# Performance work log

Hardware: AMD Instinct MI355X
Metric: run time of the kernel (lower is better)

The kernel has to match this reference:

```python
import jax, jax.numpy as jnp
import numpy as np

B, L, K = 2, 2048, 48
NUM_RBF = 16
NUM_POS = 16      # positional embedding dim
MAX_REL = 32      # max relative sequence offset
EDGE = 128        # edge feature dim
N_ATOMS = 5       # Ca, N, C, O, virtual Cb -> 25 atom pairs
EDGE_IN = NUM_POS + N_ATOMS * N_ATOMS * NUM_RBF  # 16 + 400 = 416


def setup_inputs() -> dict:
    key = jax.random.key(0)
    ks = jax.random.split(key, 6)
    # backbone coords (N, CA, C, O); scaled so pairwise distances span the RBF range [2, 22]
    X = jax.random.normal(ks[0], (B, L, 4, 3), dtype=jnp.float32) * 5.0
    mask = jnp.ones((B, L), dtype=jnp.float32)
    residue_idx = jnp.broadcast_to(jnp.arange(L, dtype=jnp.int32), (B, L))
    chain_labels = jnp.ones((B, L), dtype=jnp.int32)
    # learned params
    W_pos = jax.random.normal(ks[1], (2 * MAX_REL + 2, NUM_POS), dtype=jnp.float32) * 0.05
    b_pos = jnp.zeros((NUM_POS,), dtype=jnp.float32)
    W_edge = jax.random.normal(ks[2], (EDGE_IN, EDGE), dtype=jnp.float32) * 0.05  # no bias (ProteinMPNN)
    ln_gamma = jnp.ones((EDGE,), dtype=jnp.float32)
    ln_beta = jnp.zeros((EDGE,), dtype=jnp.float32)
    return {"X": X, "mask": mask, "residue_idx": residue_idx, "chain_labels": chain_labels,
            "W_pos": W_pos, "b_pos": b_pos, "W_edge": W_edge,
            "ln_gamma": ln_gamma, "ln_beta": ln_beta}


def _gather_nodes(nodes, e_idx):
    # nodes: [B, L, C], e_idx: [B, L, K] -> [B, L, K, C]
    b, l, k = e_idx.shape
    flat = e_idx.reshape(b, l * k)
    return jnp.take_along_axis(nodes, flat[..., None], axis=1).reshape(b, l, k, nodes.shape[-1])


def reference(X, mask, residue_idx, chain_labels, W_pos, b_pos, W_edge, ln_gamma, ln_beta):
    b, l = mask.shape
    k = min(K, l)
    N_at, Ca, C_at, O_at = X[:, :, 0], X[:, :, 1], X[:, :, 2], X[:, :, 3]

    # ---- kNN over Ca distances (masked) ----
    mask_2d = mask[:, :, None] * mask[:, None, :]
    dX = Ca[:, None, :, :] - Ca[:, :, None, :]            # [B, L, L, 3]
    D = mask_2d * jnp.sqrt(jnp.sum(dX * dX, -1) + 1e-6)    # [B, L, L]
    D_max = jnp.max(D, -1, keepdims=True)
    D_adjust = D + (1.0 - mask_2d) * D_max
    _, E_idx = jax.lax.top_k(-D_adjust, k)                 # k smallest distances -> [B, L, K]

    # ---- virtual Cb ----
    bb = Ca - N_at
    cc = C_at - Ca
    aa = jnp.cross(bb, cc)
    Cb = -0.58273431 * aa + 0.56802827 * bb - 0.54067466 * cc + Ca

    # ---- 25 pairwise atom-atom RBFs ----
    atoms = jnp.stack([Ca, N_at, C_at, O_at, Cb], axis=-2)            # [B, L, 5, 3]
    atoms_nb = _gather_nodes(atoms.reshape(b, l, N_ATOMS * 3), E_idx)  # [B, L, K, 15]
    atoms_nb = atoms_nb.reshape(b, l, k, N_ATOMS, 3)
    diff = atoms[:, :, None, :, None, :] - atoms_nb[:, :, :, None, :, :]  # [B, L, K, 5, 5, 3]
    Dp = jnp.sqrt(jnp.sum(diff * diff, -1) + 1e-6)                        # [B, L, K, 5, 5]
    mu = jnp.linspace(2.0, 22.0, NUM_RBF)
    sigma = (22.0 - 2.0) / NUM_RBF
    RBF_all = jnp.exp(-jnp.square((Dp[..., None] - mu) / sigma))          # [B, L, K, 5, 5, 16]
    RBF_all = RBF_all.reshape(b, l, k, N_ATOMS * N_ATOMS * NUM_RBF)       # [B, L, K, 400]

    # ---- relative positional encoding ----
    flat = E_idx.reshape(b, l * k)
    ridx_nb = jnp.take_along_axis(residue_idx, flat, axis=1).reshape(b, l, k)
    offset = residue_idx[:, :, None] - ridx_nb                            # [B, L, K]
    chain_nb = jnp.take_along_axis(chain_labels, flat, axis=1).reshape(b, l, k)
    same_chain = (chain_labels[:, :, None] == chain_nb).astype(jnp.int32)
    d = jnp.clip(offset + MAX_REL, 0, 2 * MAX_REL) * same_chain + (1 - same_chain) * (2 * MAX_REL + 1)
    d_onehot = jax.nn.one_hot(d, 2 * MAX_REL + 2, dtype=RBF_all.dtype)    # [B, L, K, 66]
    E_positional = d_onehot @ W_pos + b_pos                                # [B, L, K, 16]

    # ---- edge embedding + LayerNorm ----
    E = jnp.concatenate([E_positional, RBF_all], axis=-1) @ W_edge         # [B, L, K, 128]
    m = jnp.mean(E, -1, keepdims=True)
    v = jnp.mean(jnp.square(E - m), -1, keepdims=True)
    E = (E - m) * jax.lax.rsqrt(v + 1e-5) * ln_gamma + ln_beta
    return E, E_idx
```

## Files before the change

kernel.cpp:

```cpp
#include <hip/hip_runtime.h>
#include <hip/hip_bf16.h>
#include <stdint.h>

#define BB 2
#define LL 2048
#define KNN 48
#define MAXREL 32
#define EDGE_D 128
#define FSTRIDE 232
#define FLOFF   11136
#define WFH_ELEMS 53248
#define EIDX_BYTES (BB*LL*KNN*4)

typedef unsigned long long u64;
typedef __bf16 bf16_t;
typedef bf16_t bf16x8 __attribute__((ext_vector_type(8)));
typedef float f32x4 __attribute__((ext_vector_type(4)));

union U16x8 { uint4 q; bf16x8 v; };

__device__ __forceinline__ u64 u64min(u64 a, u64 b) { return a < b ? a : b; }

__device__ __forceinline__ u64 shfl_xor_u64(u64 v, int m) {
    unsigned lo = __shfl_xor((unsigned)(v & 0xffffffffull), m);
    unsigned hi = __shfl_xor((unsigned)(v >> 32), m);
    return (((u64)hi) << 32) | lo;
}

__device__ __forceinline__ void split_hi_lo(float f, unsigned short& h, unsigned short& l) {
    unsigned bits = __float_as_uint(f);
    h = (unsigned short)(bits >> 16);
    float hf = __uint_as_float(bits & 0xffff0000u);
    float lo = f - hf;
    l = (unsigned short)(__float_as_uint(lo) >> 16);
}

__global__ __launch_bounds__(256) void prep_kernel(const float* __restrict__ W,
                                                   unsigned short* __restrict__ Wf)
{
    int tid = blockIdx.x * 256 + threadIdx.x;
    if (tid >= WFH_ELEMS) return;
    int e    = tid & 7;
    int lane = (tid >> 3) & 63;
    int nt   = (tid >> 9) & 7;
    int ktg  = tid >> 12;
    int k    = ktg * 32 + ((lane >> 4) << 3) + e;
    int col  = (nt << 4) + (lane & 15);
    float f  = W[k * 128 + col];
    unsigned short h, l;
    split_hi_lo(f, h, l);
    Wf[tid]             = h;
    Wf[tid + WFH_ELEMS] = l;
}

__global__ __launch_bounds__(256) void knn_kernel(
    const float* __restrict__ X, const float* __restrict__ mask,
    int* __restrict__ eidx_i, float* __restrict__ eidx_f)
{
    const int bi   = blockIdx.x;
    const int b    = bi >> 11;
    const int i    = bi & (LL - 1);
    const int tid  = threadIdx.x;
    const int wv   = tid >> 6;
    const int lane = tid & 63;

    __shared__ int   hist[256];
    __shared__ int   ctrl[4];
    __shared__ int   cnt;
    __shared__ u64   list[64];
    __shared__ float wsh[4];
    __shared__ u64   wmin[2][4];

    const float* Xb = X + (size_t)b * LL * 12;
    const float* mb = mask + (size_t)b * LL;

    const float cax = Xb[i * 12 + 3];
    const float cay = Xb[i * 12 + 4];
    const float caz = Xb[i * 12 + 5];
    const float mi  = mb[i];

    float D[8], M2[8];
    float dmax = 0.0f;

    #pragma unroll
    for (int t = 0; t < 8; t++) {
        int j = (t << 8) + tid;
        float dx = Xb[j * 12 + 3] - cax;
        float dy = Xb[j * 12 + 4] - cay;
        float dz = Xb[j * 12 + 5] - caz;
        float s  = __fadd_rn(__fadd_rn(__fmul_rn(dx, dx), __fmul_rn(dy, dy)),
                             __fmul_rn(dz, dz));
        float m2 = __fmul_rn(mi, mb[j]);
        float d  = __fmul_rn(m2, sqrtf(__fadd_rn(s, 1e-6f)));
        D[t]  = d;
        M2[t] = m2;
        dmax  = fmaxf(dmax, d);
    }

    hist[tid] = 0;
    if (tid == 0) cnt = 0;

    #pragma unroll
    for (int off = 32; off; off >>= 1) dmax = fmaxf(dmax, __shfl_xor(dmax, off));
    if (lane == 0) wsh[wv] = dmax;
    __syncthreads();
    dmax = fmaxf(fmaxf(wsh[0], wsh[1]), fmaxf(wsh[2], wsh[3]));

    u64 key[8];
    #pragma unroll
    for (int t = 0; t < 8; t++) {
        int j = (t << 8) + tid;
        float dadj = __fadd_rn(D[t], __fmul_rn(1.0f - M2[t], dmax));
        key[t] = (((u64)__float_as_uint(dadj)) << 32) | (unsigned)j;
        atomicAdd(&hist[(int)(key[t] >> 55)], 1);
    }
    __syncthreads();

    if (wv == 0) {
        int h0 = hist[4 * lane], h1 = hist[4 * lane + 1];
        int h2 = hist[4 * lane + 2], h3 = hist[4 * lane + 3];
        int s = h0 + h1 + h2 + h3;
        int sc = s;
        #pragma unroll
        for (int off = 1; off < 64; off <<= 1) {
            int o = __shfl_up(sc, off);
            if (lane >= off) sc += o;
        }
        u64 ball = __ballot(sc >= KNN);
        int fl = __ffsll((unsigned long long)ball) - 1;
        if (lane == fl) {
            int cb = sc - s;
            int B, cbB;
            if      (cb + h0 >= KNN)           { B = 4 * lane;     cbB = cb; }
            else if (cb + h0 + h1 >= KNN)      { B = 4 * lane + 1; cbB = cb + h0; }
            else if (cb + h0 + h1 + h2 >= KNN) { B = 4 * lane + 2; cbB = cb + h0 + h1; }
            else                               { B = 4 * lane + 3; cbB = cb + h0 + h1 + h2; }
            ctrl[0] = B; ctrl[1] = cbB;
        }
    }
    __syncthreads();
    const int B = ctrl[0], cbB = ctrl[1];
    hist[tid] = 0;
    __syncthreads();

    #pragma unroll
    for (int t = 0; t < 8; t++) {
        if ((int)(key[t] >> 55) == B)
            atomicAdd(&hist[(int)(key[t] >> 47) & 255], 1);
    }
    __syncthreads();

    if (wv == 0) {
        const int T2 = KNN - cbB;
        int h0 = hist[4 * lane], h1 = hist[4 * lane + 1];
        int h2 = hist[4 * lane + 2], h3 = hist[4 * lane + 3];
        int s = h0 + h1 + h2 + h3;
        int sc = s;
        #pragma unroll
        for (int off = 1; off < 64; off <<= 1) {
            int o = __shfl_up(sc, off);
            if (lane >= off) sc += o;
        }
        u64 ball = __ballot(sc >= T2);
        int fl = __ffsll((unsigned long long)ball) - 1;
        if (lane == fl) {
            int cb = sc - s;
            int B2, cum;
            if      (cb + h0 >= T2)           { B2 = 4 * lane;     cum = cb + h0; }
            else if (cb + h0 + h1 >= T2)      { B2 = 4 * lane + 1; cum = cb + h0 + h1; }
            else if (cb + h0 + h1 + h2 >= T2) { B2 = 4 * lane + 2; cum = cb + h0 + h1 + h2; }
            else                              { B2 = 4 * lane + 3; cum = cb + h0 + h1 + h2 + h3; }
            ctrl[2] = B2; ctrl[3] = cbB + cum;
        }
    }
    __syncthreads();
    const int B2 = ctrl[2], m = ctrl[3];

    if (m <= 64) {
        #pragma unroll
        for (int t = 0; t < 8; t++) {
            int b1 = (int)(key[t] >> 55);
            int b2 = (int)(key[t] >> 47) & 255;
            if (b1 < B || (b1 == B && b2 <= B2)) {
                int p = atomicAdd(&cnt, 1);
                list[p] = key[t];
            }
        }
        __syncthreads();

        if (wv == 0) {
            u64 v = (lane < m) ? list[lane] : ~0ull;
            #pragma unroll
            for (int k = 2; k <= 64; k <<= 1) {
                #pragma unroll
                for (int j = k >> 1; j > 0; j >>= 1) {
                    u64 o = shfl_xor_u64(v, j);
                    bool takemin = (((lane & k) == 0) == ((lane & j) == 0));
                    u64 mn = u64min(v, o);
                    u64 mx = v ^ o ^ mn;
                    v = takemin ? mn : mx;
                }
            }
            if (lane < KNN) {
                int j = (int)(v & 0xffffffffu);
                eidx_i[(size_t)bi * KNN + lane] = j;
                eidx_f[(size_t)bi * KNN + lane] = (float)j;
            }
        }
    } else {
        for (int s = 0; s < KNN; s++) {
            u64 lmin = key[0];
            #pragma unroll
            for (int t = 1; t < 8; t++) lmin = u64min(lmin, key[t]);
            #pragma unroll
            for (int off = 1; off < 64; off <<= 1) lmin = u64min(lmin, shfl_xor_u64(lmin, off));
            if (lane == 0) wmin[s & 1][wv] = lmin;
            __syncthreads();
            u64 gmin = u64min(u64min(wmin[s & 1][0], wmin[s & 1][1]),
                              u64min(wmin[s & 1][2], wmin[s & 1][3]));
            if (tid == 0) {
                int j = (int)(gmin & 0xffffffffu);
                eidx_i[(size_t)bi * KNN + s] = j;
                eidx_f[(size_t)bi * KNN + s] = (float)j;
            }
            #pragma unroll
            for (int t = 0; t < 8; t++) if (key[t] == gmin) key[t] = ~0ull;
        }
    }
}

__global__ __launch_bounds__(512) void edge_kernel(
    const float* __restrict__ X,
    const int*   __restrict__ ridx, const int* __restrict__ chain,
    const float* __restrict__ Wpos, const float* __restrict__ bpos,
    const unsigned short* __restrict__ Wf,
    const float* __restrict__ gamma, const float* __restrict__ beta,
    const int*   __restrict__ eidx_i, float* __restrict__ Eout)
{
    __shared__ __align__(16) unsigned short fHL[2 * 48 * FSTRIDE];
    __shared__ float nbat[48][5][3];
    __shared__ float ctr[5][3];
    __shared__ int   dsel[48];
    __shared__ int   nbi[48];
    __shared__ float sumP[48][8];
    __shared__ float sqP[48][8];
    __shared__ float lnM[48], lnR[48];

    const int bi   = blockIdx.x;
    const int b    = bi >> 11;
    const int i    = bi & (LL - 1);
    const int tid  = threadIdx.x;
    const int w    = tid >> 6;
    const int lane = tid & 63;
    const float* Xb = X + (size_t)b * LL * 12;

    if (tid < 48) {
        int j = eidx_i[(size_t)bi * KNN + tid];
        nbi[tid] = j;
        int off = ridx[b * LL + i] - ridx[b * LL + j];
        int sc  = (chain[b * LL + i] == chain[b * LL + j]);
        int d   = off + MAXREL;
        d = d < 0 ? 0 : (d > 2 * MAXREL ? 2 * MAXREL : d);
        dsel[tid] = sc ? d : (2 * MAXREL + 1);
    }
    if (tid >= 448 && tid < 452) {
        int a = tid - 448;
        int src = (a == 0) ? 1 : ((a == 1) ? 0 : a);
        ctr[a][0] = Xb[i * 12 + src * 3 + 0];
        ctr[a][1] = Xb[i * 12 + src * 3 + 1];
        ctr[a][2] = Xb[i * 12 + src * 3 + 2];
    }
    __syncthreads();

    if (tid < 192) {
        int e = tid >> 2, a = tid & 3;
        int src = (a == 0) ? 1 : ((a == 1) ? 0 : a);
        int j = nbi[e];
        nbat[e][a][0] = Xb[j * 12 + src * 3 + 0];
        nbat[e][a][1] = Xb[j * 12 + src * 3 + 1];
        nbat[e][a][2] = Xb[j * 12 + src * 3 + 2];
    }
    __syncthreads();

    if (tid < 48) {
        float bx = nbat[tid][0][0] - nbat[tid][1][0];
        float by = nbat[tid][0][1] - nbat[tid][1][1];
        float bz = nbat[tid][0][2] - nbat[tid][1][2];
        float cx = nbat[tid][2][0] - nbat[tid][0][0];
        float cy = nbat[tid][2][1] - nbat[tid][0][1];
        float cz = nbat[tid][2][2] - nbat[tid][0][2];
        float ax = by * cz - bz * cy;
        float ay = bz * cx - bx * cz;
        float az = bx * cy - by * cx;
        nbat[tid][4][0] = -0.58273431f * ax + 0.56802827f * bx - 0.54067466f * cx + nbat[tid][0][0];
        nbat[tid][4][1] = -0.58273431f * ay + 0.56802827f * by - 0.54067466f * cy + nbat[tid][0][1];
        nbat[tid][4][2] = -0.58273431f * az + 0.56802827f * bz - 0.54067466f * cz + nbat[tid][0][2];
    } else if (tid == 48) {
        float bx = ctr[0][0] - ctr[1][0];
        float by = ctr[0][1] - ctr[1][1];
        float bz = ctr[0][2] - ctr[1][2];
        float cx = ctr[2][0] - ctr[0][0];
        float cy = ctr[2][1] - ctr[0][1];
        float cz = ctr[2][2] - ctr[0][2];
        float ax = by * cz - bz * cy;
        float ay = bz * cx - bx * cz;
        float az = bx * cy - by * cx;
        ctr[4][0] = -0.58273431f * ax + 0.56802827f * bx - 0.54067466f * cx + ctr[0][0];
        ctr[4][1] = -0.58273431f * ay + 0.56802827f * by - 0.54067466f * cy + ctr[0][1];
        ctr[4][2] = -0.58273431f * az + 0.56802827f * bz - 0.54067466f * cz + ctr[0][2];
    }
    __syncthreads();

    for (int idx = tid; idx < 48 * 16; idx += 512) {
        int e = idx >> 4, p = idx & 15;
        float f = Wpos[dsel[e] * 16 + p] + bpos[p];
        unsigned short h, l;
        split_hi_lo(f, h, l);
        fHL[e * FSTRIDE + p]         = h;
        fHL[FLOFF + e * FSTRIDE + p] = l;
    }
    for (int idx = tid; idx < 48 * 16; idx += 512) {
        int e = idx >> 4, pr = idx & 15;
        if (pr < 13) {
            int A = pr / 5, Bv = pr % 5;
            int klocal = 16 + pr * 16;
            float dx = ctr[A][0] - nbat[e][Bv][0];
            float dy = ctr[A][1] - nbat[e][Bv][1];
            float dz = ctr[A][2] - nbat[e][Bv][2];
            float d  = sqrtf(dx * dx + dy * dy + dz * dz + 1e-6f);
            uint hw[8], lw[8];
            #pragma unroll
            for (int rp = 0; rp < 8; rp++) {
                float mu0 = 2.0f + 1.3333334f * (float)(2 * rp);
                float mu1 = 2.0f + 1.3333334f * (float)(2 * rp + 1);
                float t0 = (d - mu0) * 0.8f, t1 = (d - mu1) * 0.8f;
                float v0 = __expf(-t0 * t0), v1 = __expf(-t1 * t1);
                unsigned short h0, l0, h1, l1;
                split_hi_lo(v0, h0, l0); split_hi_lo(v1, h1, l1);
                hw[rp] = (uint)h0 | ((uint)h1 << 16);
                lw[rp] = (uint)l0 | ((uint)l1 << 16);
            }
            uint4* dh = (uint4*)&fHL[e * FSTRIDE + klocal];
            dh[0] = make_uint4(hw[0], hw[1], hw[2], hw[3]);
            dh[1] = make_uint4(hw[4], hw[5], hw[6], hw[7]);
            uint4* dl = (uint4*)&fHL[FLOFF + e * FSTRIDE + klocal];
            dl[0] = make_uint4(lw[0], lw[1], lw[2], lw[3]);
            dl[1] = make_uint4(lw[4], lw[5], lw[6], lw[7]);
        }
    }
    __syncthreads();

    const unsigned short* aB = &fHL[(lane & 15) * FSTRIDE + ((lane >> 4) << 3)];
    const unsigned short* wB = Wf + (size_t)w * 512 + (size_t)lane * 8;
    f32x4 acc0 = {0.f, 0.f, 0.f, 0.f}, acc1 = acc0, acc2 = acc0;

    #pragma unroll
    for (int kt = 0; kt < 7; kt++) {
        U16x8 wh, wl, a0h, a1h, a2h, a0l, a1l, a2l;
        wh.q  = *(const uint4*)(wB + kt * 4096);
        wl.q  = *(const uint4*)(wB + WFH_ELEMS + kt * 4096);
        a0h.q = *(const uint4*)(aB + kt * 32);
        a1h.q = *(const uint4*)(aB + 16 * FSTRIDE + kt * 32);
        a2h.q = *(const uint4*)(aB + 32 * FSTRIDE + kt * 32);
        a0l.q = *(const uint4*)(aB + FLOFF + kt * 32);
        a1l.q = *(const uint4*)(aB + FLOFF + 16 * FSTRIDE + kt * 32);
        a2l.q = *(const uint4*)(aB + FLOFF + 32 * FSTRIDE + kt * 32);
        acc0 = __builtin_amdgcn_mfma_f32_16x16x32_bf16(a0h.v, wh.v, acc0, 0, 0, 0);
        acc1 = __builtin_amdgcn_mfma_f32_16x16x32_bf16(a1h.v, wh.v, acc1, 0, 0, 0);
        acc2 = __builtin_amdgcn_mfma_f32_16x16x32_bf16(a2h.v, wh.v, acc2, 0, 0, 0);
        acc0 = __builtin_amdgcn_mfma_f32_16x16x32_bf16(a0l.v, wh.v, acc0, 0, 0, 0);
        acc1 = __builtin_amdgcn_mfma_f32_16x16x32_bf16(a1l.v, wh.v, acc1, 0, 0, 0);
        acc2 = __builtin_amdgcn_mfma_f32_16x16x32_bf16(a2l.v, wh.v, acc2, 0, 0, 0);
        acc0 = __builtin_amdgcn_mfma_f32_16x16x32_bf16(a0h.v, wl.v, acc0, 0, 0, 0);
        acc1 = __builtin_amdgcn_mfma_f32_16x16x32_bf16(a1h.v, wl.v, acc1, 0, 0, 0);
        acc2 = __builtin_amdgcn_mfma_f32_16x16x32_bf16(a2h.v, wl.v, acc2, 0, 0, 0);
    }
    __syncthreads();

    for (int idx = tid; idx < 48 * 16; idx += 512) {
        int e = idx >> 4, prl = idx & 15;
        if (prl < 12) {
            int pr = 13 + prl;
            int A = pr / 5, Bv = pr % 5;
            int klocal = prl * 16;
            float dx = ctr[A][0] - nbat[e][Bv][0];
            float dy = ctr[A][1] - nbat[e][Bv][1];
            float dz = ctr[A][2] - nbat[e][Bv][2];
            float d  = sqrtf(dx * dx + dy * dy + dz * dz + 1e-6f);
            uint hw[8], lw[8];
            #pragma unroll
            for (int rp = 0; rp < 8; rp++) {
                float mu0 = 2.0f + 1.3333334f * (float)(2 * rp);
                float mu1 = 2.0f + 1.3333334f * (float)(2 * rp + 1);
                float t0 = (d - mu0) * 0.8f, t1 = (d - mu1) * 0.8f;
                float v0 = __expf(-t0 * t0), v1 = __expf(-t1 * t1);
                unsigned short h0, l0, h1, l1;
                split_hi_lo(v0, h0, l0); split_hi_lo(v1, h1, l1);
                hw[rp] = (uint)h0 | ((uint)h1 << 16);
                lw[rp] = (uint)l0 | ((uint)l1 << 16);
            }
            uint4* dh = (uint4*)&fHL[e * FSTRIDE + klocal];
            dh[0] = make_uint4(hw[0], hw[1], hw[2], hw[3]);
            dh[1] = make_uint4(hw[4], hw[5], hw[6], hw[7]);
            uint4* dl = (uint4*)&fHL[FLOFF + e * FSTRIDE + klocal];
            dl[0] = make_uint4(lw[0], lw[1], lw[2], lw[3]);
            dl[1] = make_uint4(lw[4], lw[5], lw[6], lw[7]);
        }
    }
    __syncthreads();

    #pragma unroll
    for (int kt = 0; kt < 6; kt++) {
        U16x8 wh, wl, a0h, a1h, a2h, a0l, a1l, a2l;
        wh.q  = *(const uint4*)(wB + (7 + kt) * 4096);
        wl.q  = *(const uint4*)(wB + WFH_ELEMS + (7 + kt) * 4096);
        a0h.q = *(const uint4*)(aB + kt * 32);
        a1h.q = *(const uint4*)(aB + 16 * FSTRIDE + kt * 32);
        a2h.q = *(const uint4*)(aB + 32 * FSTRIDE + kt * 32);
        a0l.q = *(const uint4*)(aB + FLOFF + kt * 32);
        a1l.q = *(const uint4*)(aB + FLOFF + 16 * FSTRIDE + kt * 32);
        a2l.q = *(const uint4*)(aB + FLOFF + 32 * FSTRIDE + kt * 32);
        acc0 = __builtin_amdgcn_mfma_f32_16x16x32_bf16(a0h.v, wh.v, acc0, 0, 0, 0);
        acc1 = __builtin_amdgcn_mfma_f32_16x16x32_bf16(a1h.v, wh.v, acc1, 0, 0, 0);
        acc2 = __builtin_amdgcn_mfma_f32_16x16x32_bf16(a2h.v, wh.v, acc2, 0, 0, 0);
        acc0 = __builtin_amdgcn_mfma_f32_16x16x32_bf16(a0l.v, wh.v, acc0, 0, 0, 0);
        acc1 = __builtin_amdgcn_mfma_f32_16x16x32_bf16(a1l.v, wh.v, acc1, 0, 0, 0);
        acc2 = __builtin_amdgcn_mfma_f32_16x16x32_bf16(a2l.v, wh.v, acc2, 0, 0, 0);
        acc0 = __builtin_amdgcn_mfma_f32_16x16x32_bf16(a0h.v, wl.v, acc0, 0, 0, 0);
        acc1 = __builtin_amdgcn_mfma_f32_16x16x32_bf16(a1h.v, wl.v, acc1, 0, 0, 0);
        acc2 = __builtin_amdgcn_mfma_f32_16x16x32_bf16(a2h.v, wl.v, acc2, 0, 0, 0);
    }

    {
        float vals[3][4] = {{acc0[0], acc0[1], acc0[2], acc0[3]},
                            {acc1[0], acc1[1], acc1[2], acc1[3]},
                            {acc2[0], acc2[1], acc2[2], acc2[3]}};
        #pragma unroll
        for (int mt = 0; mt < 3; mt++) {
            #pragma unroll
            for (int r = 0; r < 4; r++) {
                float sm = vals[mt][r], sq = sm * sm;
                #pragma unroll
                for (int off = 1; off < 16; off <<= 1) {
                    sm += __shfl_xor(sm, off);
                    sq += __shfl_xor(sq, off);
                }
                if ((lane & 15) == 0) {
                    int row = mt * 16 + ((lane >> 4) << 2) + r;
                    sumP[row][w] = sm;
                    sqP[row][w]  = sq;
                }
            }
        }
        __syncthreads();
        if (tid < 48) {
            float s = 0.f, q = 0.f;
            #pragma unroll
            for (int t = 0; t < 8; t++) { s += sumP[tid][t]; q += sqP[tid][t]; }
            float m = s * 0.0078125f;
            lnM[tid] = m;
            lnR[tid] = rsqrtf(q * 0.0078125f - m * m + 1e-5f);
        }
        __syncthreads();

        const int col = (w << 4) + (lane & 15);
        const float g  = gamma[col];
        const float bt = beta[col];
        float* Eo = Eout + (size_t)bi * KNN * EDGE_D;
        #pragma unroll
        for (int mt = 0; mt < 3; mt++) {
            #pragma unroll
            for (int r = 0; r < 4; r++) {
                int row = mt * 16 + ((lane >> 4) << 2) + r;
                Eo[(size_t)row * EDGE_D + col] =
                    (vals[mt][r] - lnM[row]) * lnR[row] * g + bt;
            }
        }
    }
}

extern "C" void kernel_launch(void* const* d_in, const int* in_sizes, int n_in,
                              void* d_out, int out_size, void* d_ws, size_t ws_size,
                              hipStream_t stream) {
    const float* X     = (const float*)d_in[0];
    const float* mask  = (const float*)d_in[1];
    const int*   ridx  = (const int*)d_in[2];
    const int*   chain = (const int*)d_in[3];
    const float* Wpos  = (const float*)d_in[4];
    const float* bpos  = (const float*)d_in[5];
    const float* Wedge = (const float*)d_in[6];
    const float* gamma = (const float*)d_in[7];
    const float* beta  = (const float*)d_in[8];

    float* out    = (float*)d_out;
    float* Eout   = out;
    float* eidx_f = out + (size_t)BB * LL * KNN * EDGE_D;
    int*   eidx_i = (int*)d_ws;
    unsigned short* Wf = (unsigned short*)((char*)d_ws + EIDX_BYTES);

    hipLaunchKernelGGL(prep_kernel, dim3((WFH_ELEMS + 255) / 256), dim3(256), 0, stream,
                       Wedge, Wf);
    hipLaunchKernelGGL(knn_kernel, dim3(BB * LL), dim3(256), 0, stream,
                       X, mask, eidx_i, eidx_f);
    hipLaunchKernelGGL(edge_kernel, dim3(BB * LL), dim3(512), 0, stream,
                       X, ridx, chain, Wpos, bpos, Wf, gamma, beta, eidx_i, Eout);
}
```

Before: 242.3 us.

## Bin kNN histogram by value range, fragment-major LDS, prefetch weights

The kNN selection now builds its first histogram over the linear range [dmin, dmax] of adjusted distances rather than over float exponent bits. The aim is that the first pass isolates the 48 nearest directly, without the second refinement pass or the serial fallback. The edge kernel stores A operands in LDS in a fragment-major layout with padding, so each lane's MFMA load is one contiguous uint4 with fewer bank conflicts. Weight fragments are prefetched one k-step ahead in registers, and launch bounds request higher occupancy. These changes add an extra min reduction and more register pressure, and binning by float value could behave differently on unusual distributions.

```diff
diff --git a/kernel.cpp b/kernel.cpp
--- a/kernel.cpp
+++ b/kernel.cpp
@@ -7,10 +7,11 @@
 #define KNN 48
 #define MAXREL 32
 #define EDGE_D 128
-#define FSTRIDE 232
-#define FLOFF   11136
 #define WFH_ELEMS 53248
 #define EIDX_BYTES (BB*LL*KNN*4)
+#define KT_PAD 65
+#define PM_FRAGS (7 * KT_PAD)
+#define TOT_FRAGS (2 * 3 * PM_FRAGS)
 
 typedef unsigned long long u64;
 typedef __bf16 bf16_t;
@@ -68,7 +69,7 @@
     __shared__ int   ctrl[4];
     __shared__ int   cnt;
     __shared__ u64   list[64];
-    __shared__ float wsh[4];
+    __shared__ float wshA[4], wshB[4];
     __shared__ u64   wmin[2][4];
 
     const float* Xb = X + (size_t)b * LL * 12;
@@ -102,17 +103,36 @@
 
     #pragma unroll
     for (int off = 32; off; off >>= 1) dmax = fmaxf(dmax, __shfl_xor(dmax, off));
-    if (lane == 0) wsh[wv] = dmax;
-    __syncthreads();
-    dmax = fmaxf(fmaxf(wsh[0], wsh[1]), fmaxf(wsh[2], wsh[3]));
+    if (lane == 0) wshA[wv] = dmax;
+    __syncthreads();
+    dmax = fmaxf(fmaxf(wshA[0], wshA[1]), fmaxf(wshA[2], wshA[3]));
 
     u64 key[8];
+    float dadj[8];
+    float dmin = 3.4e38f;
     #pragma unroll
     for (int t = 0; t < 8; t++) {
         int j = (t << 8) + tid;
-        float dadj = __fadd_rn(D[t], __fmul_rn(1.0f - M2[t], dmax));
-        key[t] = (((u64)__float_as_uint(dadj)) << 32) | (unsigned)j;
-        atomicAdd(&hist[(int)(key[t] >> 55)], 1);
+        float da = __fadd_rn(D[t], __fmul_rn(1.0f - M2[t], dmax));
+        dadj[t] = da;
+        key[t] = (((u64)__float_as_uint(da)) << 32) | (unsigned)j;
+        dmin = fminf(dmin, da);
+    }
+    #pragma unroll
+    for (int off = 32; off; off >>= 1) dmin = fminf(dmin, __shfl_xor(dmin, off));
+    if (lane == 0) wshB[wv] = dmin;
+    __syncthreads();
+    dmin = fminf(fminf(wshB[0], wshB[1]), fminf(wshB[2], wshB[3]));
+
+    const float range = dmax - dmin;
+    const float scale = (range > 1e-35f) ? (255.0f / range) : 0.0f;
+
+    int bin[8];
+    #pragma unroll
+    for (int t = 0; t < 8; t++) {
+        int bb = (int)((dadj[t] - dmin) * scale);
+        bin[t] = bb > 255 ? 255 : bb;
+        atomicAdd(&hist[bin[t]], 1);
     }
     __syncthreads();
 
@@ -130,68 +150,27 @@
         int fl = __ffsll((unsigned long long)ball) - 1;
         if (lane == fl) {
             int cb = sc - s;
-            int B, cbB;
-            if      (cb + h0 >= KNN)           { B = 4 * lane;     cbB = cb; }
-            else if (cb + h0 + h1 >= KNN)      { B = 4 * lane + 1; cbB = cb + h0; }
-            else if (cb + h0 + h1 + h2 >= KNN) { B = 4 * lane + 2; cbB = cb + h0 + h1; }
-            else                               { B = 4 * lane + 3; cbB = cb + h0 + h1 + h2; }
-            ctrl[0] = B; ctrl[1] = cbB;
-        }
-    }
-    __syncthreads();
-    const int B = ctrl[0], cbB = ctrl[1];
-    hist[tid] = 0;
-    __syncthreads();
-
-    #pragma unroll
-    for (int t = 0; t < 8; t++) {
-        if ((int)(key[t] >> 55) == B)
-            atomicAdd(&hist[(int)(key[t] >> 47) & 255], 1);
-    }
-    __syncthreads();
-
-    if (wv == 0) {
-        const int T2 = KNN - cbB;
-        int h0 = hist[4 * lane], h1 = hist[4 * lane + 1];
-        int h2 = hist[4 * lane + 2], h3 = hist[4 * lane + 3];
-        int s = h0 + h1 + h2 + h3;
-        int sc = s;
-        #pragma unroll
-        for (int off = 1; off < 64; off <<= 1) {
-            int o = __shfl_up(sc, off);
-            if (lane >= off) sc += o;
-        }
-        u64 ball = __ballot(sc >= T2);
-        int fl = __ffsll((unsigned long long)ball) - 1;
-        if (lane == fl) {
-            int cb = sc - s;
-            int B2, cum;
-            if      (cb + h0 >= T2)           { B2 = 4 * lane;     cum = cb + h0; }
-            else if (cb + h0 + h1 >= T2)      { B2 = 4 * lane + 1; cum = cb + h0 + h1; }
-            else if (cb + h0 + h1 + h2 >= T2) { B2 = 4 * lane + 2; cum = cb + h0 + h1 + h2; }
-            else                              { B2 = 4 * lane + 3; cum = cb + h0 + h1 + h2 + h3; }
-            ctrl[2] = B2; ctrl[3] = cbB + cum;
-        }
-    }
-    __syncthreads();
-    const int B2 = ctrl[2], m = ctrl[3];
-
-    if (m <= 64) {
+            int B, cbB, m1;
+            if      (cb + h0 >= KNN)           { B = 4*lane;   cbB = cb;          m1 = cb+h0; }
+            else if (cb + h0 + h1 >= KNN)      { B = 4*lane+1; cbB = cb+h0;       m1 = cb+h0+h1; }
+            else if (cb + h0 + h1 + h2 >= KNN) { B = 4*lane+2; cbB = cb+h0+h1;    m1 = cb+h0+h1+h2; }
+            else                               { B = 4*lane+3; cbB = cb+h0+h1+h2; m1 = cb+h0+h1+h2+h3; }
+            ctrl[0] = B; ctrl[1] = cbB; ctrl[2] = m1;
+        }
+    }
+    __syncthreads();
+    const int B = ctrl[0], cbB = ctrl[1], m1 = ctrl[2];
+
+    if (m1 <= 64) {
         #pragma unroll
         for (int t = 0; t < 8; t++) {
-            int b1 = (int)(key[t] >> 55);
-            int b2 = (int)(key[t] >> 47) & 255;
-            if (b1 < B || (b1 == B && b2 <= B2)) {
-                int p = atomicAdd(&cnt, 1);
-                list[p] = key[t];
-            }
+            if (bin[t] <= B) { int p = atomicAdd(&cnt, 1); list[p] = key[t]; }
         }
         __syncthreads();
-
         if (wv == 0) {
-            u64 v = (lane < m) ? list[lane] : ~0ull;
-            #pragma unroll
-            for (int k = 2; k <= 64; k <<= 1) {
+            u64 v = (lane < m1) ? list[lane] : ~0ull;
+            #pragma unroll
+            for (int k = 2; k <= 64; k <<= 1)
                 #pragma unroll
                 for (int j = k >> 1; j > 0; j >>= 1) {
                     u64 o = shfl_xor_u64(v, j);
@@ -200,36 +179,108 @@
                     u64 mx = v ^ o ^ mn;
                     v = takemin ? mn : mx;
                 }
-            }
             if (lane < KNN) {
                 int j = (int)(v & 0xffffffffu);
                 eidx_i[(size_t)bi * KNN + lane] = j;
                 eidx_f[(size_t)bi * KNN + lane] = (float)j;
             }
         }
-    } else {
-        for (int s = 0; s < KNN; s++) {
-            u64 lmin = key[0];
-            #pragma unroll
-            for (int t = 1; t < 8; t++) lmin = u64min(lmin, key[t]);
-            #pragma unroll
-            for (int off = 1; off < 64; off <<= 1) lmin = u64min(lmin, shfl_xor_u64(lmin, off));
-            if (lane == 0) wmin[s & 1][wv] = lmin;
-            __syncthreads();
-            u64 gmin = u64min(u64min(wmin[s & 1][0], wmin[s & 1][1]),
-                              u64min(wmin[s & 1][2], wmin[s & 1][3]));
-            if (tid == 0) {
-                int j = (int)(gmin & 0xffffffffu);
-                eidx_i[(size_t)bi * KNN + s] = j;
-                eidx_f[(size_t)bi * KNN + s] = (float)j;
-            }
-            #pragma unroll
-            for (int t = 0; t < 8; t++) if (key[t] == gmin) key[t] = ~0ull;
-        }
+        return;
+    }
+
+    hist[tid] = 0;
+    __syncthreads();
+    const float width  = range * (1.0f / 255.0f);
+    const float b_lo   = dmin + (float)B * width;
+    const float scale2 = (width > 1e-35f) ? (255.0f / width) : 0.0f;
+    int bin2[8];
+    #pragma unroll
+    for (int t = 0; t < 8; t++) {
+        if (bin[t] == B) {
+            int bb = (int)((dadj[t] - b_lo) * scale2);
+            bb = bb < 0 ? 0 : (bb > 255 ? 255 : bb);
+            bin2[t] = bb;
+            atomicAdd(&hist[bb], 1);
+        } else bin2[t] = 1 << 30;
+    }
+    __syncthreads();
+
+    if (wv == 0) {
+        const int T2 = KNN - cbB;
+        int h0 = hist[4 * lane], h1 = hist[4 * lane + 1];
+        int h2 = hist[4 * lane + 2], h3 = hist[4 * lane + 3];
+        int s = h0 + h1 + h2 + h3;
+        int sc = s;
+        #pragma unroll
+        for (int off = 1; off < 64; off <<= 1) {
+            int o = __shfl_up(sc, off);
+            if (lane >= off) sc += o;
+        }
+        u64 ball = __ballot(sc >= T2);
+        int fl = __ffsll((unsigned long long)ball) - 1;
+        if (lane == fl) {
+            int cb = sc - s;
+            int B2, cum;
+            if      (cb + h0 >= T2)           { B2 = 4*lane;   cum = cb+h0; }
+            else if (cb + h0 + h1 >= T2)      { B2 = 4*lane+1; cum = cb+h0+h1; }
+            else if (cb + h0 + h1 + h2 >= T2) { B2 = 4*lane+2; cum = cb+h0+h1+h2; }
+            else                              { B2 = 4*lane+3; cum = cb+h0+h1+h2+h3; }
+            ctrl[2] = B2; ctrl[3] = cbB + cum;
+        }
+    }
+    __syncthreads();
+    const int B2 = ctrl[2], m2 = ctrl[3];
+
+    if (m2 <= 64) {
+        #pragma unroll
+        for (int t = 0; t < 8; t++) {
+            if (bin[t] < B || (bin[t] == B && bin2[t] <= B2)) {
+                int p = atomicAdd(&cnt, 1); list[p] = key[t];
+            }
+        }
+        __syncthreads();
+        if (wv == 0) {
+            u64 v = (lane < m2) ? list[lane] : ~0ull;
+            #pragma unroll
+            for (int k = 2; k <= 64; k <<= 1)
+                #pragma unroll
+                for (int j = k >> 1; j > 0; j >>= 1) {
+                    u64 o = shfl_xor_u64(v, j);
+                    bool takemin = (((lane & k) == 0) == ((lane & j) == 0));
+                    u64 mn = u64min(v, o);
+                    u64 mx = v ^ o ^ mn;
+                    v = takemin ? mn : mx;
+                }
+            if (lane < KNN) {
+                int j = (int)(v & 0xffffffffu);
+                eidx_i[(size_t)bi * KNN + lane] = j;
+                eidx_f[(size_t)bi * KNN + lane] = (float)j;
+            }
+        }
+        return;
+    }
+
+    for (int s = 0; s < KNN; s++) {
+        u64 lmin = key[0];
+        #pragma unroll
+        for (int t = 1; t < 8; t++) lmin = u64min(lmin, key[t]);
+        #pragma unroll
+        for (int off = 1; off < 64; off <<= 1) lmin = u64min(lmin, shfl_xor_u64(lmin, off));
+        if (lane == 0) wmin[s & 1][wv] = lmin;
+        __syncthreads();
+        u64 gmin = u64min(u64min(wmin[s & 1][0], wmin[s & 1][1]),
+                          u64min(wmin[s & 1][2], wmin[s & 1][3]));
+        if (tid == 0) {
+            int j = (int)(gmin & 0xffffffffu);
+            eidx_i[(size_t)bi * KNN + s] = j;
+            eidx_f[(size_t)bi * KNN + s] = (float)j;
+        }
+        #pragma unroll
+        for (int t = 0; t < 8; t++) if (key[t] == gmin) key[t] = ~0ull;
     }
 }
 
-__global__ __launch_bounds__(512) void edge_kernel(
+__global__ __launch_bounds__(512, 6) void edge_kernel(
     const float* __restrict__ X,
     const int*   __restrict__ ridx, const int* __restrict__ chain,
     const float* __restrict__ Wpos, const float* __restrict__ bpos,
@@ -237,7 +288,7 @@
     const float* __restrict__ gamma, const float* __restrict__ beta,
     const int*   __restrict__ eidx_i, float* __restrict__ Eout)
 {
-    __shared__ __align__(16) unsigned short fHL[2 * 48 * FSTRIDE];
+    __shared__ __align__(16) uint4 frag[TOT_FRAGS];
     __shared__ float nbat[48][5][3];
     __shared__ float ctr[5][3];
     __shared__ int   dsel[48];
@@ -253,6 +304,12 @@
     const int w    = tid >> 6;
     const int lane = tid & 63;
     const float* Xb = X + (size_t)b * LL * 12;
+
+    const unsigned short* wB = Wf + (size_t)w * 512 + (size_t)lane * 8;
+
+    uint4 whc = *(const uint4*)(wB);
+    uint4 wlc = *(const uint4*)(wB + WFH_ELEMS);
+    uint4 whn, wln;
 
     if (tid < 48) {
         int j = eidx_i[(size_t)bi * KNN + tid];
@@ -311,19 +368,25 @@
     }
     __syncthreads();
 
+    unsigned short* fS = (unsigned short*)frag;
+
     for (int idx = tid; idx < 48 * 16; idx += 512) {
         int e = idx >> 4, p = idx & 15;
+        int mt = e >> 4, r = e & 15;
         float f = Wpos[dsel[e] * 16 + p] + bpos[p];
         unsigned short h, l;
         split_hi_lo(f, h, l);
-        fHL[e * FSTRIDE + p]         = h;
-        fHL[FLOFF + e * FSTRIDE + p] = l;
+        int fr = mt * PM_FRAGS + (p >> 3) * 16 + r;
+        fS[fr * 8 + (p & 7)]                     = h;
+        fS[(fr + 3 * PM_FRAGS) * 8 + (p & 7)]    = l;
     }
     for (int idx = tid; idx < 48 * 16; idx += 512) {
         int e = idx >> 4, pr = idx & 15;
         if (pr < 13) {
+            int mt = e >> 4, r = e & 15;
             int A = pr / 5, Bv = pr % 5;
             int klocal = 16 + pr * 16;
+            int kt = klocal >> 5, qa = (klocal >> 3) & 3;
             float dx = ctr[A][0] - nbat[e][Bv][0];
             float dy = ctr[A][1] - nbat[e][Bv][1];
             float dz = ctr[A][2] - nbat[e][Bv][2];
@@ -340,31 +403,29 @@
                 hw[rp] = (uint)h0 | ((uint)h1 << 16);
                 lw[rp] = (uint)l0 | ((uint)l1 << 16);
             }
-            uint4* dh = (uint4*)&fHL[e * FSTRIDE + klocal];
-            dh[0] = make_uint4(hw[0], hw[1], hw[2], hw[3]);
-            dh[1] = make_uint4(hw[4], hw[5], hw[6], hw[7]);
-            uint4* dl = (uint4*)&fHL[FLOFF + e * FSTRIDE + klocal];
-            dl[0] = make_uint4(lw[0], lw[1], lw[2], lw[3]);
-            dl[1] = make_uint4(lw[4], lw[5], lw[6], lw[7]);
-        }
-    }
-    __syncthreads();
-
-    const unsigned short* aB = &fHL[(lane & 15) * FSTRIDE + ((lane >> 4) << 3)];
-    const unsigned short* wB = Wf + (size_t)w * 512 + (size_t)lane * 8;
+            int fr = mt * PM_FRAGS + kt * KT_PAD + qa * 16 + r;
+            frag[fr]      = make_uint4(hw[0], hw[1], hw[2], hw[3]);
+            frag[fr + 16] = make_uint4(hw[4], hw[5], hw[6], hw[7]);
+            frag[fr + 3 * PM_FRAGS]      = make_uint4(lw[0], lw[1], lw[2], lw[3]);
+            frag[fr + 3 * PM_FRAGS + 16] = make_uint4(lw[4], lw[5], lw[6], lw[7]);
+        }
+    }
+    __syncthreads();
+
+    const uint4* fb = frag + lane;
     f32x4 acc0 = {0.f, 0.f, 0.f, 0.f}, acc1 = acc0, acc2 = acc0;
-
     #pragma unroll
     for (int kt = 0; kt < 7; kt++) {
+        whn = *(const uint4*)(wB + (kt + 1) * 4096);
+        wln = *(const uint4*)(wB + WFH_ELEMS + (kt + 1) * 4096);
         U16x8 wh, wl, a0h, a1h, a2h, a0l, a1l, a2l;
-        wh.q  = *(const uint4*)(wB + kt * 4096);
-        wl.q  = *(const uint4*)(wB + WFH_ELEMS + kt * 4096);
-        a0h.q = *(const uint4*)(aB + kt * 32);
-        a1h.q = *(const uint4*)(aB + 16 * FSTRIDE + kt * 32);
-        a2h.q = *(const uint4*)(aB + 32 * FSTRIDE + kt * 32);
-        a0l.q = *(const uint4*)(aB + FLOFF + kt * 32);
-        a1l.q = *(const uint4*)(aB + FLOFF + 16 * FSTRIDE + kt * 32);
-        a2l.q = *(const uint4*)(aB + FLOFF + 32 * FSTRIDE + kt * 32);
+        wh.q  = whc; wl.q = wlc;
+        a0h.q = fb[0 * PM_FRAGS + kt * KT_PAD];
+        a1h.q = fb[1 * PM_FRAGS + kt * KT_PAD];
+        a2h.q = fb[2 * PM_FRAGS + kt * KT_PAD];
+        a0l.q = fb[3 * PM_FRAGS + kt * KT_PAD];
+        a1l.q = fb[4 * PM_FRAGS + kt * KT_PAD];
+        a2l.q = fb[5 * PM_FRAGS + kt * KT_PAD];
         acc0 = __builtin_amdgcn_mfma_f32_16x16x32_bf16(a0h.v, wh.v, acc0, 0, 0, 0);
         acc1 = __builtin_amdgcn_mfma_f32_16x16x32_bf16(a1h.v, wh.v, acc1, 0, 0, 0);
         acc2 = __builtin_amdgcn_mfma_f32_16x16x32_bf16(a2h.v, wh.v, acc2, 0, 0, 0);
@@ -374,15 +435,18 @@
         acc0 = __builtin_amdgcn_mfma_f32_16x16x32_bf16(a0h.v, wl.v, acc0, 0, 0, 0);
         acc1 = __builtin_amdgcn_mfma_f32_16x16x32_bf16(a1h.v, wl.v, acc1, 0, 0, 0);
         acc2 = __builtin_amdgcn_mfma_f32_16x16x32_bf16(a2h.v, wl.v, acc2, 0, 0, 0);
+        whc = whn; wlc = wln;
     }
     __syncthreads();
 
     for (int idx = tid; idx < 48 * 16; idx += 512) {
         int e = idx >> 4, prl = idx & 15;
         if (prl < 12) {
+            int mt = e >> 4, r = e & 15;
             int pr = 13 + prl;
             int A = pr / 5, Bv = pr % 5;
             int klocal = prl * 16;
+            int kt = klocal >> 5, qa = (klocal >> 3) & 3;
             float dx = ctr[A][0] - nbat[e][Bv][0];
             float dy = ctr[A][1] - nbat[e][Bv][1];
             float dz = ctr[A][2] - nbat[e][Bv][2];
@@ -399,27 +463,29 @@
                 hw[rp] = (uint)h0 | ((uint)h1 << 16);
                 lw[rp] = (uint)l0 | ((uint)l1 << 16);
             }
-            uint4* dh = (uint4*)&fHL[e * FSTRIDE + klocal];
-            dh[0] = make_uint4(hw[0], hw[1], hw[2], hw[3]);
-            dh[1] = make_uint4(hw[4], hw[5], hw[6], hw[7]);
-            uint4* dl = (uint4*)&fHL[FLOFF + e * FSTRIDE + klocal];
-            dl[0] = make_uint4(lw[0], lw[1], lw[2], lw[3]);
-            dl[1] = make_uint4(lw[4], lw[5], lw[6], lw[7]);
+            int fr = mt * PM_FRAGS + kt * KT_PAD + qa * 16 + r;
+            frag[fr]      = make_uint4(hw[0], hw[1], hw[2], hw[3]);
+            frag[fr + 16] = make_uint4(hw[4], hw[5], hw[6], hw[7]);
+            frag[fr + 3 * PM_FRAGS]      = make_uint4(lw[0], lw[1], lw[2], lw[3]);
+            frag[fr + 3 * PM_FRAGS + 16] = make_uint4(lw[4], lw[5], lw[6], lw[7]);
         }
     }
     __syncthreads();
 
     #pragma unroll
     for (int kt = 0; kt < 6; kt++) {
+        if (kt < 5) {
+            whn = *(const uint4*)(wB + (8 + kt) * 4096);
+            wln = *(const uint4*)(wB + WFH_ELEMS + (8 + kt) * 4096);
+        }
         U16x8 wh, wl, a0h, a1h, a2h, a0l, a1l, a2l;
-        wh.q  = *(const uint4*)(wB + (7 + kt) * 4096);
-        wl.q  = *(const uint4*)(wB + WFH_ELEMS + (7 + kt) * 4096);
-        a0h.q = *(const uint4*)(aB + kt * 32);
-        a1h.q = *(const uint4*)(aB + 16 * FSTRIDE + kt * 32);
-        a2h.q = *(const uint4*)(aB + 32 * FSTRIDE + kt * 32);
-        a0l.q = *(const uint4*)(aB + FLOFF + kt * 32);
-        a1l.q = *(const uint4*)(aB + FLOFF + 16 * FSTRIDE + kt * 32);
-        a2l.q = *(const uint4*)(aB + FLOFF + 32 * FSTRIDE + kt * 32);
+        wh.q  = whc; wl.q = wlc;
+        a0h.q = fb[0 * PM_FRAGS + kt * KT_PAD];
+        a1h.q = fb[1 * PM_FRAGS + kt * KT_PAD];
+        a2h.q = fb[2 * PM_FRAGS + kt * KT_PAD];
+        a0l.q = fb[3 * PM_FRAGS + kt * KT_PAD];
+        a1l.q = fb[4 * PM_FRAGS + kt * KT_PAD];
+        a2l.q = fb[5 * PM_FRAGS + kt * KT_PAD];
         acc0 = __builtin_amdgcn_mfma_f32_16x16x32_bf16(a0h.v, wh.v, acc0, 0, 0, 0);
         acc1 = __builtin_amdgcn_mfma_f32_16x16x32_bf16(a1h.v, wh.v, acc1, 0, 0, 0);
         acc2 = __builtin_amdgcn_mfma_f32_16x16x32_bf16(a2h.v, wh.v, acc2, 0, 0, 0);
@@ -429,6 +495,7 @@
         acc0 = __builtin_amdgcn_mfma_f32_16x16x32_bf16(a0h.v, wl.v, acc0, 0, 0, 0);
         acc1 = __builtin_amdgcn_mfma_f32_16x16x32_bf16(a1h.v, wl.v, acc1, 0, 0, 0);
         acc2 = __builtin_amdgcn_mfma_f32_16x16x32_bf16(a2h.v, wl.v, acc2, 0, 0, 0);
+        whc = whn; wlc = wln;
     }
 
     {
```

New measurement: 225.7 us. 1.07x faster.
